# Performance work log

Hardware: AMD Instinct MI355X
Metric: run time of the kernel (lower is better)

## Reference

```python
import jax, jax.numpy as jnp
import numpy as np

D = 768
H = 12
HD = D // H
NEG = -10000.0
EPS = 1e-12


def setup_inputs() -> dict:
    key = jax.random.key(0)
    ks = jax.random.split(key, 8)
    B, S = 4, 1024
    xavier = lambda k: jax.random.normal(k, (D, D), dtype=jnp.float32) * np.sqrt(2.0 / (D + D))
    return {
        "embeddings": jax.random.normal(ks[0], (B, S, D), dtype=jnp.float32),
        "padding_mask": jnp.ones((B, S), dtype=jnp.float32),
        "wq_w": xavier(ks[1]), "wq_b": jnp.zeros((D,), jnp.float32),
        "wk_w": xavier(ks[2]), "wk_b": jnp.zeros((D,), jnp.float32),
        "wv_w": xavier(ks[3]), "wv_b": jnp.zeros((D,), jnp.float32),
        "wo_w": xavier(ks[4]), "wo_b": jnp.zeros((D,), jnp.float32),
        "ln_g": jnp.ones((D,), jnp.float32), "ln_b": jnp.zeros((D,), jnp.float32),
    }


def reference(embeddings, padding_mask, wq_w, wq_b, wk_w, wk_b, wv_w, wv_b, wo_w, wo_b, ln_g, ln_b):
    B, S, _ = embeddings.shape
    # QKV projections (torch Linear: x @ W^T + b), split heads -> [B,H,S,HD]
    split = lambda t: t.reshape(B, S, H, HD).transpose(0, 2, 1, 3)
    q = split(embeddings @ wq_w.T + wq_b)
    k = split(embeddings @ wk_w.T + wk_b)
    v = split(embeddings @ wv_w.T + wv_b)
    # NOTE: original scales by sqrt(embedding_dim), not sqrt(per-head dim)
    attn = jnp.einsum("bhqd,bhkd->bhqk", q, k) / jnp.sqrt(jnp.float32(D))
    # additive padding mask, then causal masked_fill (set, not add)
    attn = attn + ((1.0 - padding_mask)[:, None, None, :] * NEG)
    causal = jnp.tril(jnp.ones((S, S), dtype=jnp.float32))
    attn = jnp.where(causal[None, None] == 0, NEG, attn)
    attn_probs = jax.nn.softmax(attn, axis=-1)  # dropout is identity at inference
    ctx = jnp.einsum("bhqk,bhkd->bhqd", attn_probs, v)
    ctx = ctx.transpose(0, 2, 1, 3).reshape(B, S, D)
    attn_out = ctx @ wo_w.T + wo_b  # keep_prob = 1.0 -> no rescale
    # residual + LayerNorm(eps=1e-12)
    x = attn_out + embeddings
    mu = jnp.mean(x, axis=-1, keepdims=True)
    var = jnp.mean((x - mu) ** 2, axis=-1, keepdims=True)
    normed = (x - mu) * jax.lax.rsqrt(var + EPS) * ln_g + ln_b
    return (normed, attn_probs)
```

## Files before the change

kernel.cpp:

```cpp
#include <hip/hip_runtime.h>
#include <hip/hip_bf16.h>

typedef __bf16 bf16x8 __attribute__((ext_vector_type(8)));
typedef float  f32x4  __attribute__((ext_vector_type(4)));

#define NEGC (-10000.0f)
#define GLDS(src, dst) __builtin_amdgcn_global_load_lds(
#undef GLDS

static __device__ __forceinline__ void glds16(const __bf16* src, __bf16* dst) {
    __builtin_amdgcn_global_load_lds((const __attribute__((address_space(1))) unsigned int*)src,
                                     (__attribute__((address_space(3))) unsigned int*)dst, 16, 0, 0);
}

__global__ __launch_bounds__(256) void cvt_bf16(const float* __restrict__ in,
                                                __bf16* __restrict__ out, int n8) {
    int i = blockIdx.x * 256 + threadIdx.x;
    if (i >= n8) return;
    f32x4 a = *(const f32x4*)(in + (size_t)i * 8);
    f32x4 b = *(const f32x4*)(in + (size_t)i * 8 + 4);
    bf16x8 o;
    o[0] = (__bf16)a[0]; o[1] = (__bf16)a[1]; o[2] = (__bf16)a[2]; o[3] = (__bf16)a[3];
    o[4] = (__bf16)b[0]; o[5] = (__bf16)b[1]; o[6] = (__bf16)b[2]; o[7] = (__bf16)b[3];
    *(bf16x8*)(out + (size_t)i * 8) = o;
}

__global__ __launch_bounds__(256) void cvt_w4(const float* __restrict__ q, const float* __restrict__ k,
                                              const float* __restrict__ v, const float* __restrict__ o,
                                              __bf16* __restrict__ dst) {
    int blk = blockIdx.x;
    int which = blk / 288;
    const float* src = which == 0 ? q : which == 1 ? k : which == 2 ? v : o;
    int i = (blk - which * 288) * 256 + threadIdx.x;
    f32x4 a = *(const f32x4*)(src + (size_t)i * 8);
    f32x4 b = *(const f32x4*)(src + (size_t)i * 8 + 4);
    bf16x8 o8;
    o8[0] = (__bf16)a[0]; o8[1] = (__bf16)a[1]; o8[2] = (__bf16)a[2]; o8[3] = (__bf16)a[3];
    o8[4] = (__bf16)b[0]; o8[5] = (__bf16)b[1]; o8[6] = (__bf16)b[2]; o8[7] = (__bf16)b[3];
    *(bf16x8*)(dst + (size_t)which * 589824 + (size_t)i * 8) = o8;
}

template<int MODE>
__global__ __launch_bounds__(256) void gemm128(
    const __bf16* __restrict__ A, const __bf16* __restrict__ Bw,
    const float* __restrict__ b0, const float* __restrict__ b1, const float* __restrict__ b2,
    __bf16* __restrict__ O0, __bf16* __restrict__ O1, __bf16* __restrict__ O2,
    const float* __restrict__ res, float* __restrict__ Yout)
{
    __shared__ __align__(16) __bf16 As[128 * 32];
    __shared__ __align__(16) __bf16 Bs[128 * 32];
    const int K = 768;
    int tid = threadIdx.x;
    int l = tid & 63, w = tid >> 6;
    int lo = l & 15, hi = l >> 4;
    int m0 = blockIdx.x * 128, n0 = blockIdx.y * 128;
    int wr = w >> 1, wc = w & 1;

    f32x4 acc[4][4] = {};

    int srow = w * 16 + (l >> 2);
    int scol = (l & 3) * 8;
    const __bf16* gA = A + (size_t)(m0 + srow) * K + scol;
    const __bf16* gB = Bw + (size_t)(n0 + srow) * K + scol;
    __bf16* lA = As + w * 512 + l * 8;
    __bf16* lB = Bs + w * 512 + l * 8;

    for (int k0 = 0; k0 < K; k0 += 32) {
        if (k0) __syncthreads();
        glds16(gA + k0, lA);
        glds16(gA + (size_t)64 * K + k0, lA + 2048);
        glds16(gB + k0, lB);
        glds16(gB + (size_t)64 * K + k0, lB + 2048);
        __syncthreads();

        bf16x8 af[4], bfr[4];
#pragma unroll
        for (int mi = 0; mi < 4; mi++)
            af[mi] = *(const bf16x8*)(As + (wr * 64 + mi * 16 + lo) * 32 + hi * 8);
#pragma unroll
        for (int ni = 0; ni < 4; ni++)
            bfr[ni] = *(const bf16x8*)(Bs + (wc * 64 + ni * 16 + lo) * 32 + hi * 8);
#pragma unroll
        for (int mi = 0; mi < 4; mi++)
#pragma unroll
            for (int ni = 0; ni < 4; ni++)
                acc[mi][ni] = __builtin_amdgcn_mfma_f32_16x16x32_bf16(af[mi], bfr[ni], acc[mi][ni], 0, 0, 0);
    }

    if constexpr (MODE == 0) {
        int which = n0 / 768;
        const float* bias = which == 0 ? b0 : (which == 1 ? b1 : b2);
        __bf16* O = which == 0 ? O0 : (which == 1 ? O1 : O2);
        int nbase = n0 - which * 768;
#pragma unroll
        for (int mi = 0; mi < 4; mi++)
#pragma unroll
            for (int ni = 0; ni < 4; ni++) {
                int within = nbase + wc * 64 + ni * 16 + lo;
                float bv = bias[within];
                int h = within >> 6, d = within & 63;
#pragma unroll
                for (int i = 0; i < 4; i++) {
                    int m = m0 + wr * 64 + mi * 16 + hi * 4 + i;
                    int bb = m >> 10, s = m & 1023;
                    O[(size_t)((bb * 12 + h) * 1024 + s) * 64 + d] = (__bf16)(acc[mi][ni][i] + bv);
                }
            }
    } else {
#pragma unroll
        for (int mi = 0; mi < 4; mi++)
#pragma unroll
            for (int ni = 0; ni < 4; ni++) {
                int n = n0 + wc * 64 + ni * 16 + lo;
                float bv = b0[n];
#pragma unroll
                for (int i = 0; i < 4; i++) {
                    int m = m0 + wr * 64 + mi * 16 + hi * 4 + i;
                    size_t idx = (size_t)m * 768 + n;
                    Yout[idx] = acc[mi][ni][i] + bv + res[idx];
                }
            }
    }
}

__global__ __launch_bounds__(256) void attn_kernel(
    const __bf16* __restrict__ Q, const __bf16* __restrict__ K, const __bf16* __restrict__ V,
    const float* __restrict__ pmask, float* __restrict__ Pout, __bf16* __restrict__ ctx)
{
    int bh = blockIdx.x;
    int b = bh / 12, h = bh - b * 12;
    int y = blockIdx.y;
    int q0 = y * 64;
    int tid = threadIdx.x, l = tid & 63, w = tid >> 6;
    int lo = l & 15, hi = l >> 4;
    int qw = q0 + w * 16;

    const __bf16* Qh = Q + (size_t)bh * 65536;
    const __bf16* Kh = K + (size_t)bh * 65536;
    const __bf16* Vh = V + (size_t)bh * 65536;
    float* Ph = Pout + (size_t)bh * 1048576;
    const float* pm = pmask + b * 1024;

    __shared__ __align__(16) __bf16 Ks[2][64][64];
    __shared__ __align__(16) __bf16 vt[2][64][72];
    __shared__ __align__(16) __bf16 plds[4][16][72];

    const float scale = 0.036084391824351615f;

    bf16x8 qf0 = *(const bf16x8*)(Qh + (size_t)(qw + lo) * 64 + hi * 8);
    bf16x8 qf1 = *(const bf16x8*)(Qh + (size_t)(qw + lo) * 64 + 32 + hi * 8);

    int srow = tid >> 3;
    int scb  = (tid & 7) ^ (srow & 7);
    __bf16* ldst0 = &Ks[0][0][0] + tid * 8;

#define STAGE_K(buf, kt)  do {                                             \
        glds16(Kh + (size_t)((kt) * 64 + srow) * 64 + scb * 8,             \
               ldst0 + (buf) * 4096);                                      \
        glds16(Kh + (size_t)((kt) * 64 + 32 + srow) * 64 + scb * 8,        \
               ldst0 + (buf) * 4096 + 2048);                               \
    } while (0)

#define KFRAG(buf, kn, dh) \
    (*(const bf16x8*)(&Ks[buf][(kn) * 16 + lo][(((dh) * 4 + hi) ^ (lo & 7)) * 8]))

    float lsum[4] = {};
    STAGE_K(0, 0);
    __syncthreads();
    for (int kt = 0; kt <= y; kt++) {
        int cur = kt & 1;
        if (kt < y) STAGE_K(cur ^ 1, kt + 1);
        int k0 = kt * 64;
        float pad[4];
#pragma unroll
        for (int kn = 0; kn < 4; kn++) pad[kn] = (1.0f - pm[k0 + kn * 16 + lo]) * NEGC;
        f32x4 s[4] = {};
        __builtin_amdgcn_s_setprio(1);
#pragma unroll
        for (int kn = 0; kn < 4; kn++) {
            s[kn] = __builtin_amdgcn_mfma_f32_16x16x32_bf16(qf0, KFRAG(cur, kn, 0), s[kn], 0, 0, 0);
            s[kn] = __builtin_amdgcn_mfma_f32_16x16x32_bf16(qf1, KFRAG(cur, kn, 1), s[kn], 0, 0, 0);
        }
        __builtin_amdgcn_s_setprio(0);
#pragma unroll
        for (int kn = 0; kn < 4; kn++) {
            int c = k0 + kn * 16 + lo;
#pragma unroll
            for (int i = 0; i < 4; i++) {
                int r = qw + hi * 4 + i;
                float a = s[kn][i] * scale + pad[kn];
                if (c > r) a = NEGC;
                lsum[i] += __expf(a);
            }
        }
        __syncthreads();
    }

    float invl[4];
#pragma unroll
    for (int i = 0; i < 4; i++) {
        float s = lsum[i];
        s += __shfl_xor(s, 1);
        s += __shfl_xor(s, 2);
        s += __shfl_xor(s, 4);
        s += __shfl_xor(s, 8);
        invl[i] = 1.0f / s;
    }

    int vrow = tid >> 2, vcol = (tid & 3) * 16;
    bf16x8 va, vb;
    {
        STAGE_K(0, 0);
        const __bf16* vp = Vh + (size_t)vrow * 64 + vcol;
        va = *(const bf16x8*)vp; vb = *(const bf16x8*)(vp + 8);
#pragma unroll
        for (int j = 0; j < 8; j++) vt[0][vcol + j][vrow] = va[j];
#pragma unroll
        for (int j = 0; j < 8; j++) vt[0][vcol + 8 + j][vrow] = vb[j];
        if (y > 0) {
            const __bf16* vp1 = Vh + (size_t)(64 + vrow) * 64 + vcol;
            va = *(const bf16x8*)vp1; vb = *(const bf16x8*)(vp1 + 8);
        }
        __syncthreads();
    }

    f32x4 cacc[4] = {};
    for (int kt = 0; kt <= y; kt++) {
        int cur = kt & 1;
        if (kt < y) STAGE_K(cur ^ 1, kt + 1);
        int k0 = kt * 64;
        float pad[4];
#pragma unroll
        for (int kn = 0; kn < 4; kn++) pad[kn] = (1.0f - pm[k0 + kn * 16 + lo]) * NEGC;
        f32x4 s[4] = {};
        __builtin_amdgcn_s_setprio(1);
#pragma unroll
        for (int kn = 0; kn < 4; kn++) {
            s[kn] = __builtin_amdgcn_mfma_f32_16x16x32_bf16(qf0, KFRAG(cur, kn, 0), s[kn], 0, 0, 0);
            s[kn] = __builtin_amdgcn_mfma_f32_16x16x32_bf16(qf1, KFRAG(cur, kn, 1), s[kn], 0, 0, 0);
        }
        __builtin_amdgcn_s_setprio(0);
#pragma unroll
        for (int kn = 0; kn < 4; kn++) {
            int c = k0 + kn * 16 + lo;
#pragma unroll
            for (int i = 0; i < 4; i++) {
                int r = qw + hi * 4 + i;
                float a = s[kn][i] * scale + pad[kn];
                if (c > r) a = NEGC;
                float p = __expf(a) * invl[i];
                Ph[(size_t)r * 1024 + c] = p;
                plds[w][hi * 4 + i][kn * 16 + lo] = (__bf16)p;
            }
        }
        __builtin_amdgcn_s_setprio(1);
#pragma unroll
        for (int ks = 0; ks < 2; ks++) {
            bf16x8 pf = *(const bf16x8*)(&plds[w][lo][ks * 32 + hi * 8]);
#pragma unroll
            for (int dt = 0; dt < 4; dt++) {
                bf16x8 vf = *(const bf16x8*)(&vt[cur][dt * 16 + lo][ks * 32 + hi * 8]);
                cacc[dt] = __builtin_amdgcn_mfma_f32_16x16x32_bf16(pf, vf, cacc[dt], 0, 0, 0);
            }
        }
        __builtin_amdgcn_s_setprio(0);
        if (kt < y) {
#pragma unroll
            for (int j = 0; j < 8; j++) vt[cur ^ 1][vcol + j][vrow] = va[j];
#pragma unroll
            for (int j = 0; j < 8; j++) vt[cur ^ 1][vcol + 8 + j][vrow] = vb[j];
            if (kt + 1 < y) {
                const __bf16* vp = Vh + (size_t)((kt + 2) * 64 + vrow) * 64 + vcol;
                va = *(const bf16x8*)vp; vb = *(const bf16x8*)(vp + 8);
            }
        }
        __syncthreads();
    }

#pragma unroll
    for (int dt = 0; dt < 4; dt++) {
#pragma unroll
        for (int i = 0; i < 4; i++) {
            int m = b * 1024 + qw + hi * 4 + i;
            int n = h * 64 + dt * 16 + lo;
            ctx[(size_t)m * 768 + n] = (__bf16)cacc[dt][i];
        }
    }

    for (int c = (y + 1) * 64 + lo * 4; c < 1024; c += 64) {
#pragma unroll
        for (int i = 0; i < 4; i++) {
            f32x4 z = {};
            *(f32x4*)(Ph + (size_t)(qw + hi * 4 + i) * 1024 + c) = z;
        }
    }
#undef STAGE_K
#undef KFRAG
}

__global__ __launch_bounds__(256) void ln_kernel(
    const float* __restrict__ Y, const float* __restrict__ g, const float* __restrict__ bta,
    float* __restrict__ out)
{
    int row = blockIdx.x * 4 + (threadIdx.x >> 6);
    int l = threadIdx.x & 63;
    const float* yr = Y + (size_t)row * 768;
    f32x4 v0 = *(const f32x4*)(yr + l * 4);
    f32x4 v1 = *(const f32x4*)(yr + 256 + l * 4);
    f32x4 v2 = *(const f32x4*)(yr + 512 + l * 4);
    float s = v0[0] + v0[1] + v0[2] + v0[3] + v1[0] + v1[1] + v1[2] + v1[3]
            + v2[0] + v2[1] + v2[2] + v2[3];
#pragma unroll
    for (int m = 1; m < 64; m <<= 1) s += __shfl_xor(s, m);
    float mu = s * (1.0f / 768.0f);
    float ss = 0.0f;
#pragma unroll
    for (int j = 0; j < 4; j++) {
        float d0 = v0[j] - mu, d1 = v1[j] - mu, d2 = v2[j] - mu;
        ss += d0 * d0 + d1 * d1 + d2 * d2;
    }
#pragma unroll
    for (int m = 1; m < 64; m <<= 1) ss += __shfl_xor(ss, m);
    float r = rsqrtf(ss * (1.0f / 768.0f) + 1e-12f);
    float* orow = out + (size_t)row * 768;
#pragma unroll
    for (int c = 0; c < 3; c++) {
        f32x4 v = (c == 0) ? v0 : ((c == 1) ? v1 : v2);
        int col = c * 256 + l * 4;
        f32x4 gg = *(const f32x4*)(g + col);
        f32x4 bb = *(const f32x4*)(bta + col);
        f32x4 o;
#pragma unroll
        for (int j = 0; j < 4; j++) o[j] = (v[j] - mu) * r * gg[j] + bb[j];
        *(f32x4*)(orow + col) = o;
    }
}

extern "C" void kernel_launch(void* const* d_in, const int* in_sizes, int n_in,
                              void* d_out, int out_size, void* d_ws, size_t ws_size,
                              hipStream_t stream)
{
    const float* emb   = (const float*)d_in[0];
    const float* pmask = (const float*)d_in[1];
    const float* wq = (const float*)d_in[2];  const float* bq = (const float*)d_in[3];
    const float* wk = (const float*)d_in[4];  const float* bk = (const float*)d_in[5];
    const float* wv = (const float*)d_in[6];  const float* bv = (const float*)d_in[7];
    const float* wo = (const float*)d_in[8];  const float* bo = (const float*)d_in[9];
    const float* lng = (const float*)d_in[10]; const float* lnb = (const float*)d_in[11];

    __bf16* Xb   = (__bf16*)d_ws;
    __bf16* Wall = Xb + 4096 * 768;
    __bf16* Qb   = Wall + 4 * 589824;
    __bf16* Kb   = Qb + 3145728;
    __bf16* Vb   = Kb + 3145728;
    __bf16* Cb   = Vb + 3145728;
    float*  Yf   = (float*)(Cb + 3145728);

    float* normed = (float*)d_out;
    float* probs  = normed + (size_t)4096 * 768;

    cvt_bf16<<<1536, 256, 0, stream>>>(emb, Xb, 393216);
    cvt_w4<<<1152, 256, 0, stream>>>(wq, wk, wv, wo, Wall);

    gemm128<0><<<dim3(32, 18), 256, 0, stream>>>(Xb, Wall, bq, bk, bv, Qb, Kb, Vb, nullptr, nullptr);
    attn_kernel<<<dim3(48, 16), 256, 0, stream>>>(Qb, Kb, Vb, pmask, probs, Cb);
    gemm128<1><<<dim3(32, 6), 256, 0, stream>>>(Cb, Wall + 3 * 589824, bo, nullptr, nullptr,
                                                nullptr, nullptr, nullptr, emb, Yf);
    ln_kernel<<<1024, 256, 0, stream>>>(Yf, lng, lnb, normed);
}
```

Measured before the change: 128.1 us.

## Load K fragments directly from global memory instead of LDS double-buffering

Removes the LDS staging of K tiles (global_load_lds double buffer plus per-tile barriers) in both attention passes. Each lane now reads its K MFMA fragments straight from global memory, relying on L1/L2 caching since all four waves read the same K tile. The launch bounds also request 4 blocks per SM to raise occupancy, and the padding-mask loads move after the MFMAs. In exchange, K traffic to cache is duplicated across waves and global-load latency is exposed, with no prefetch, before each tile's MFMAs.

```diff
diff --git a/kernel.cpp b/kernel.cpp
--- a/kernel.cpp
+++ b/kernel.cpp
@@ -5,8 +5,6 @@
 typedef float  f32x4  __attribute__((ext_vector_type(4)));
 
 #define NEGC (-10000.0f)
-#define GLDS(src, dst) __builtin_amdgcn_global_load_lds(
-#undef GLDS
 
 static __device__ __forceinline__ void glds16(const __bf16* src, __bf16* dst) {
     __builtin_amdgcn_global_load_lds((const __attribute__((address_space(1))) unsigned int*)src,
@@ -123,7 +121,7 @@
     }
 }
 
-__global__ __launch_bounds__(256) void attn_kernel(
+__global__ __launch_bounds__(256, 4) void attn_kernel(
     const __bf16* __restrict__ Q, const __bf16* __restrict__ K, const __bf16* __restrict__ V,
     const float* __restrict__ pmask, float* __restrict__ Pout, __bf16* __restrict__ ctx)
 {
@@ -141,7 +139,6 @@
     float* Ph = Pout + (size_t)bh * 1048576;
     const float* pm = pmask + b * 1024;
 
-    __shared__ __align__(16) __bf16 Ks[2][64][64];
     __shared__ __align__(16) __bf16 vt[2][64][72];
     __shared__ __align__(16) __bf16 plds[4][16][72];
 
@@ -150,38 +147,25 @@
     bf16x8 qf0 = *(const bf16x8*)(Qh + (size_t)(qw + lo) * 64 + hi * 8);
     bf16x8 qf1 = *(const bf16x8*)(Qh + (size_t)(qw + lo) * 64 + 32 + hi * 8);
 
-    int srow = tid >> 3;
-    int scb  = (tid & 7) ^ (srow & 7);
-    __bf16* ldst0 = &Ks[0][0][0] + tid * 8;
-
-#define STAGE_K(buf, kt)  do {                                             \
-        glds16(Kh + (size_t)((kt) * 64 + srow) * 64 + scb * 8,             \
-               ldst0 + (buf) * 4096);                                      \
-        glds16(Kh + (size_t)((kt) * 64 + 32 + srow) * 64 + scb * 8,        \
-               ldst0 + (buf) * 4096 + 2048);                               \
-    } while (0)
-
-#define KFRAG(buf, kn, dh) \
-    (*(const bf16x8*)(&Ks[buf][(kn) * 16 + lo][(((dh) * 4 + hi) ^ (lo & 7)) * 8]))
+    const __bf16* kbase = Kh + (size_t)lo * 64 + hi * 8;
 
     float lsum[4] = {};
-    STAGE_K(0, 0);
-    __syncthreads();
     for (int kt = 0; kt <= y; kt++) {
-        int cur = kt & 1;
-        if (kt < y) STAGE_K(cur ^ 1, kt + 1);
         int k0 = kt * 64;
-        float pad[4];
-#pragma unroll
-        for (int kn = 0; kn < 4; kn++) pad[kn] = (1.0f - pm[k0 + kn * 16 + lo]) * NEGC;
+        const __bf16* kb = kbase + (size_t)k0 * 64;
         f32x4 s[4] = {};
         __builtin_amdgcn_s_setprio(1);
 #pragma unroll
         for (int kn = 0; kn < 4; kn++) {
-            s[kn] = __builtin_amdgcn_mfma_f32_16x16x32_bf16(qf0, KFRAG(cur, kn, 0), s[kn], 0, 0, 0);
-            s[kn] = __builtin_amdgcn_mfma_f32_16x16x32_bf16(qf1, KFRAG(cur, kn, 1), s[kn], 0, 0, 0);
+            bf16x8 ka = *(const bf16x8*)(kb + kn * 1024);
+            bf16x8 kc = *(const bf16x8*)(kb + kn * 1024 + 32);
+            s[kn] = __builtin_amdgcn_mfma_f32_16x16x32_bf16(qf0, ka, s[kn], 0, 0, 0);
+            s[kn] = __builtin_amdgcn_mfma_f32_16x16x32_bf16(qf1, kc, s[kn], 0, 0, 0);
         }
         __builtin_amdgcn_s_setprio(0);
+        float pad[4];
+#pragma unroll
+        for (int kn = 0; kn < 4; kn++) pad[kn] = (1.0f - pm[k0 + kn * 16 + lo]) * NEGC;
 #pragma unroll
         for (int kn = 0; kn < 4; kn++) {
             int c = k0 + kn * 16 + lo;
@@ -193,7 +177,6 @@
                 lsum[i] += __expf(a);
             }
         }
-        __syncthreads();
     }
 
     float invl[4];
@@ -210,7 +193,6 @@
     int vrow = tid >> 2, vcol = (tid & 3) * 16;
     bf16x8 va, vb;
     {
-        STAGE_K(0, 0);
         const __bf16* vp = Vh + (size_t)vrow * 64 + vcol;
         va = *(const bf16x8*)vp; vb = *(const bf16x8*)(vp + 8);
 #pragma unroll
@@ -227,19 +209,21 @@
     f32x4 cacc[4] = {};
     for (int kt = 0; kt <= y; kt++) {
         int cur = kt & 1;
-        if (kt < y) STAGE_K(cur ^ 1, kt + 1);
         int k0 = kt * 64;
-        float pad[4];
-#pragma unroll
-        for (int kn = 0; kn < 4; kn++) pad[kn] = (1.0f - pm[k0 + kn * 16 + lo]) * NEGC;
+        const __bf16* kb = kbase + (size_t)k0 * 64;
         f32x4 s[4] = {};
         __builtin_amdgcn_s_setprio(1);
 #pragma unroll
         for (int kn = 0; kn < 4; kn++) {
-            s[kn] = __builtin_amdgcn_mfma_f32_16x16x32_bf16(qf0, KFRAG(cur, kn, 0), s[kn], 0, 0, 0);
-            s[kn] = __builtin_amdgcn_mfma_f32_16x16x32_bf16(qf1, KFRAG(cur, kn, 1), s[kn], 0, 0, 0);
+            bf16x8 ka = *(const bf16x8*)(kb + kn * 1024);
+            bf16x8 kc = *(const bf16x8*)(kb + kn * 1024 + 32);
+            s[kn] = __builtin_amdgcn_mfma_f32_16x16x32_bf16(qf0, ka, s[kn], 0, 0, 0);
+            s[kn] = __builtin_amdgcn_mfma_f32_16x16x32_bf16(qf1, kc, s[kn], 0, 0, 0);
         }
         __builtin_amdgcn_s_setprio(0);
+        float pad[4];
+#pragma unroll
+        for (int kn = 0; kn < 4; kn++) pad[kn] = (1.0f - pm[k0 + kn * 16 + lo]) * NEGC;
 #pragma unroll
         for (int kn = 0; kn < 4; kn++) {
             int c = k0 + kn * 16 + lo;
@@ -294,8 +278,6 @@
             *(f32x4*)(Ph + (size_t)(qw + hi * 4 + i) * 1024 + c) = z;
         }
     }
-#undef STAGE_K
-#undef KFRAG
 }
 
 __global__ __launch_bounds__(256) void ln_kernel(
```

Measured after the change: 165.3 us. 1.29x slower.
